# Kernel tuning notes

Hardware: AMD Instinct MI355X
Metric: run time of the kernel (lower is better)

## Reference

```python
import jax, jax.numpy as jnp
import numpy as np


def gcn_conv(x, src, dst, W, b, n_nodes):
    """PyG-style GCNConv: add self-loops, symmetric deg^-1/2 normalization,
    linear transform, scatter-add aggregation to dst, then bias."""
    loop = jnp.arange(n_nodes, dtype=src.dtype)
    s = jnp.concatenate([src, loop])
    d = jnp.concatenate([dst, loop])
    deg = jax.ops.segment_sum(jnp.ones_like(d, x.dtype), d, num_segments=n_nodes)
    dinv = jax.lax.rsqrt(deg)  # deg >= 1 due to self-loops
    norm = dinv[s] * dinv[d]  # [E+N]
    h = x @ W.T  # [N, out]
    msg = h[s] * norm[:, None]  # [E+N, out]
    return jax.ops.segment_sum(msg, d, num_segments=n_nodes) + b


def setup_inputs() -> dict:
    key = jax.random.key(0)
    k = jax.random.split(key, 6)
    N, E, IN, HID, OUT = 100000, 1600000, 128, 128, 64
    x = jax.random.normal(k[0], (N, IN), dtype=jnp.float32)
    edge_index = jax.random.randint(k[1], (2, E), 0, N, dtype=jnp.int64)
    W1 = jax.random.normal(k[2], (HID, IN), dtype=jnp.float32) * 0.05
    b1 = jnp.zeros((HID,), dtype=jnp.float32)
    W2 = jax.random.normal(k[3], (OUT, HID), dtype=jnp.float32) * 0.05
    b2 = jnp.zeros((OUT,), dtype=jnp.float32)
    return {"x": x, "W1": W1, "b1": b1, "W2": W2, "b2": b2, "edge_index": edge_index}


def reference(x, W1, b1, W2, b2, edge_index):
    n_nodes = x.shape[0]
    src, dst = edge_index[0], edge_index[1]
    h = jax.nn.relu(gcn_conv(x, src, dst, W1, b1, n_nodes))
    return gcn_conv(h, src, dst, W2, b2, n_nodes)
```

## Files before the change

kernel.cpp:

```cpp
#include <hip/hip_runtime.h>
#include <hip/hip_bf16.h>


#define IN_F  128
#define HID_F 128
#define OUT_F 64

#define NPB     128
#define MAXBKT  1024
#define CHUNK   2048
#define CAP     4096
#define SLAB    4096

typedef __bf16 bf16_t;
typedef __bf16 bf16x4 __attribute__((ext_vector_type(4)));
typedef __bf16 bf16x8 __attribute__((ext_vector_type(8)));
typedef float  f32x2  __attribute__((ext_vector_type(2)));
typedef float  f32x4  __attribute__((ext_vector_type(4)));
typedef unsigned u32x2 __attribute__((ext_vector_type(2)));
typedef unsigned u32x4 __attribute__((ext_vector_type(4)));

__global__ __launch_bounds__(256) void k_hist(const int* __restrict__ dst, int E,
                                              int* __restrict__ chunkhist, int NBKT,
                                              int pchunks,
                                              const float* __restrict__ W1s,
                                              const float* __restrict__ W2s,
                                              bf16_t* __restrict__ Wdst,
                                              int n1, int n2,
                                              int* __restrict__ bcur) {
    if ((int)blockIdx.x >= pchunks) {
        int i = (blockIdx.x - pchunks) * 256 + threadIdx.x;
        if (i < n1) Wdst[i] = (bf16_t)W1s[i];
        else if (i < n1 + n2) Wdst[i] = (bf16_t)W2s[i - n1];
        else if (i < n1 + n2 + NBKT) bcur[i - n1 - n2] = (i - n1 - n2) * SLAB;
        return;
    }
    __shared__ int cnt[MAXBKT];
    for (int i = threadIdx.x; i < NBKT; i += 256) cnt[i] = 0;
    __syncthreads();
    int base = blockIdx.x * CHUNK;
    for (int i = threadIdx.x; i < CHUNK; i += 256) {
        int e = base + i;
        if (e < E) atomicAdd(&cnt[dst[e] >> 7], 1);
    }
    __syncthreads();
    int* ch = chunkhist + (size_t)blockIdx.x * MAXBKT;
    for (int i = threadIdx.x; i < NBKT; i += 256) ch[i] = cnt[i];
}

__global__ __launch_bounds__(256) void k_part(const int* __restrict__ src,
                                              const int* __restrict__ dst, int E,
                                              int* __restrict__ bcur,
                                              const int* __restrict__ chunkhist,
                                              unsigned* __restrict__ part, int NBKT) {
    __shared__ int cnt[MAXBKT];
    __shared__ int base[MAXBKT];
    const int* ch = chunkhist + (size_t)blockIdx.x * MAXBKT;
    int off = (int)((blockIdx.x * 331u) % (unsigned)NBKT);
    for (int j = threadIdx.x; j < NBKT; j += 256) {
        int i = j + off; if (i >= NBKT) i -= NBKT;
        int c = ch[i];
        base[i] = c ? atomicAdd(&bcur[i], c) : 0;
        cnt[i] = 0;
    }
    __syncthreads();
    int cbase = blockIdx.x * CHUNK;
    for (int i = threadIdx.x; i < CHUNK; i += 256) {
        int e = cbase + i;
        if (e < E) {
            int d = dst[e];
            int b = d >> 7;
            int lp = atomicAdd(&cnt[b], 1);
            part[base[b] + lp] = (unsigned)src[e] | ((unsigned)(d & 127) << 17);
        }
    }
}

__global__ __launch_bounds__(256) void k_bucket(const unsigned* __restrict__ part,
                                                const int* __restrict__ bcur,
                                                int2* __restrict__ off2,
                                                int* __restrict__ col,
                                                float* __restrict__ dinv, int N) {
    __shared__ int lcnt[NPB];
    __shared__ int lexc[NPB];
    __shared__ int lcur[NPB];
    __shared__ int stage[CAP];
    int b = blockIdx.x;
    int t = threadIdx.x;
    int node0 = b * NPB;
    int nb = min(NPB, N - node0);
    int e0s = b * SLAB;
    int cnt = bcur[b] - e0s;
    if (t < NPB) lcnt[t] = 0;
    __syncthreads();
    for (int i = t; i < cnt; i += 256)
        atomicAdd(&lcnt[part[e0s + i] >> 17], 1);
    __syncthreads();
    if (t < NPB) lexc[t] = (lcnt[t] + 7) & ~7;
    __syncthreads();
    for (int ofs = 1; ofs < NPB; ofs <<= 1) {
        int add = (t >= ofs && t < NPB) ? lexc[t - ofs] : 0;
        __syncthreads();
        if (t < NPB) lexc[t] += add;
        __syncthreads();
    }
    if (t < NPB) {
        int pc = (lcnt[t] + 7) & ~7;
        int ex = lexc[t] - pc;
        lcur[t] = ex;
        if (t < nb) {
            off2[node0 + t] = make_int2(e0s + ex, e0s + ex + pc);
            dinv[node0 + t] = rsqrtf((float)lcnt[t] + 1.0f);
        }
    }
    __syncthreads();
    for (int i = t; i < cnt; i += 256) {
        unsigned p = part[e0s + i];
        int dl = p >> 17;
        int sv = (int)(p & 0x1FFFF);
        int lp = atomicAdd(&lcur[dl], 1);
        if (lp < CAP) stage[lp] = sv;
        else col[e0s + lp] = sv;
    }
    __syncthreads();
    if (t < NPB) {
        int en = lexc[t];
        for (int i = lcur[t]; i < en; i++) {
            if (i < CAP) stage[i] = N; else col[e0s + i] = N;
        }
    }
    __syncthreads();
    int tot = lexc[NPB - 1];
    for (int i = t; i < tot && i < CAP; i += 256) col[e0s + i] = stage[i];
}

template <int NCOL, typename TIN>
__global__ __launch_bounds__(256) void k_gemm_mfma(const TIN* __restrict__ X,
                                                   const bf16_t* __restrict__ W,
                                                   const float* __restrict__ scale,
                                                   bf16_t* __restrict__ H, int N) {
    constexpr int CT = NCOL / 16;
    int wv = threadIdx.x >> 6, lane = threadIdx.x & 63;
    int quad = lane >> 4, l16 = lane & 15;
    int row0 = blockIdx.x * 128 + wv * 32;
    f32x4 acc[2][CT] = {};
#pragma unroll
    for (int ks = 0; ks < 4; ks++) {
        int k0 = ks * 32 + quad * 8;
        bf16x8 a[2];
#pragma unroll
        for (int rt = 0; rt < 2; rt++) {
            int r = row0 + rt * 16 + l16;
            if (r >= N) r = N - 1;
            const TIN* p = X + (size_t)r * 128 + k0;
            if constexpr (sizeof(TIN) == 4) {
                f32x4 x0 = *(const f32x4*)p;
                f32x4 x1 = *(const f32x4*)(p + 4);
                bf16x8 tt;
                tt[0] = (bf16_t)x0[0]; tt[1] = (bf16_t)x0[1];
                tt[2] = (bf16_t)x0[2]; tt[3] = (bf16_t)x0[3];
                tt[4] = (bf16_t)x1[0]; tt[5] = (bf16_t)x1[1];
                tt[6] = (bf16_t)x1[2]; tt[7] = (bf16_t)x1[3];
                a[rt] = tt;
            } else {
                a[rt] = *(const bf16x8*)p;
            }
        }
#pragma unroll
        for (int ct = 0; ct < CT; ct++) {
            bf16x8 bfrag = *(const bf16x8*)(W + (size_t)(ct * 16 + l16) * 128 + k0);
#pragma unroll
            for (int rt = 0; rt < 2; rt++)
                acc[rt][ct] = __builtin_amdgcn_mfma_f32_16x16x32_bf16(a[rt], bfrag, acc[rt][ct], 0, 0, 0);
        }
    }
#pragma unroll
    for (int rt = 0; rt < 2; rt++)
#pragma unroll
        for (int r4 = 0; r4 < 4; r4++) {
            int r = row0 + rt * 16 + quad * 4 + r4;
            if (r < N) {
                float sc = scale[r];
#pragma unroll
                for (int ct = 0; ct < CT; ct++)
                    H[(size_t)r * NCOL + ct * 16 + l16] = (bf16_t)(sc * acc[rt][ct][r4]);
            } else if (r == N) {
#pragma unroll
                for (int ct = 0; ct < CT; ct++)
                    H[(size_t)N * NCOL + ct * 16 + l16] = (bf16_t)0.f;
            }
        }
}

template <int ROWE>
__device__ __forceinline__ void gather8(const bf16_t* __restrict__ hp,
                                        const int* __restrict__ col, int e,
                                        u32x4* w) {
    int4 c0 = *(const int4*)(col + e);
    int4 c1 = *(const int4*)(col + e + 4);
    w[0] = *(const u32x4*)(hp + (unsigned)c0.x * (unsigned)ROWE);
    w[1] = *(const u32x4*)(hp + (unsigned)c0.y * (unsigned)ROWE);
    w[2] = *(const u32x4*)(hp + (unsigned)c0.z * (unsigned)ROWE);
    w[3] = *(const u32x4*)(hp + (unsigned)c0.w * (unsigned)ROWE);
    w[4] = *(const u32x4*)(hp + (unsigned)c1.x * (unsigned)ROWE);
    w[5] = *(const u32x4*)(hp + (unsigned)c1.y * (unsigned)ROWE);
    w[6] = *(const u32x4*)(hp + (unsigned)c1.z * (unsigned)ROWE);
    w[7] = *(const u32x4*)(hp + (unsigned)c1.w * (unsigned)ROWE);
}

__device__ __forceinline__ void accum8(const u32x4* w, f32x2* a2) {
#pragma unroll
    for (int u = 0; u < 8; u++)
#pragma unroll
        for (int k = 0; k < 4; k++) {
            f32x2 v;
            v.x = __uint_as_float(w[u][k] << 16);
            v.y = __uint_as_float(w[u][k] & 0xffff0000u);
            a2[k] += v;
        }
}

__global__ __launch_bounds__(256) void k_agg_gemm(const bf16_t* __restrict__ h,
                                                  const int2* __restrict__ off2,
                                                  const int* __restrict__ col,
                                                  const float* __restrict__ dinv,
                                                  const float* __restrict__ bias,
                                                  const bf16_t* __restrict__ W2,
                                                  bf16_t* __restrict__ h2, int N) {
    __shared__ float hl[16][132];
    __shared__ float dl[16];
    int lane = threadIdx.x & 63;
    int wv = threadIdx.x >> 6;
    int g = lane >> 4, fl = lane & 15;
    int node0 = blockIdx.x * 16;
    int node = node0 + wv * 4 + g;
    bool alive = node < N;
    int f = fl * 8;
    const bf16_t* hp = h + f;
    f32x2 a2[4] = {};
    float di = 0.f;
    if (alive) {
        u32x4 ws = *(const u32x4*)(hp + (unsigned)node * 128u);
        int2 oe = off2[node];
        di = dinv[node];
#pragma unroll
        for (int k = 0; k < 4; k++) {
            f32x2 v;
            v.x = __uint_as_float(ws[k] << 16);
            v.y = __uint_as_float(ws[k] & 0xffff0000u);
            a2[k] = v;
        }
        u32x4 w[8];
        for (int e = oe.x; e < oe.y; e += 8) {
            gather8<128>(hp, col, e, w);
            accum8(w, a2);
        }
    }
    f32x4 b0 = *(const f32x4*)(bias + f);
    f32x4 b1 = *(const f32x4*)(bias + f + 4);
    int lr = wv * 4 + g;
#pragma unroll
    for (int j = 0; j < 8; j++) {
        float bv = (j < 4) ? b0[j] : b1[j - 4];
        float val = a2[j >> 1][j & 1] * di + bv;
        hl[lr][f + j] = fmaxf(val, 0.f);
    }
    if (fl == 0) dl[lr] = di;
    __syncthreads();

    int quad = lane >> 4, l16 = lane & 15;
    f32x4 c4 = {0.f, 0.f, 0.f, 0.f};
#pragma unroll
    for (int ks = 0; ks < 4; ks++) {
        int k0 = ks * 32 + quad * 8;
        bf16x8 afr;
#pragma unroll
        for (int j = 0; j < 8; j++) afr[j] = (bf16_t)hl[l16][k0 + j];
        bf16x8 bfr = *(const bf16x8*)(W2 + (size_t)(wv * 16 + l16) * 128 + k0);
        c4 = __builtin_amdgcn_mfma_f32_16x16x32_bf16(afr, bfr, c4, 0, 0, 0);
    }
#pragma unroll
    for (int r4 = 0; r4 < 4; r4++) {
        int rr = quad * 4 + r4;
        int gn = node0 + rr;
        if (gn < N)
            h2[(size_t)gn * 64 + wv * 16 + l16] = (bf16_t)(dl[rr] * c4[r4]);
    }
    if (blockIdx.x == 0 && threadIdx.x < 32)
        ((unsigned*)h2)[(size_t)N * 32 + threadIdx.x] = 0u;
}

template <int ROWE, int LPN, bool RELU, typename TOUT>
__global__ __launch_bounds__(256) void k_agg(const bf16_t* __restrict__ h,
                                             const int2* __restrict__ off2,
                                             const int* __restrict__ col,
                                             const float* __restrict__ dinv,
                                             const float* __restrict__ bias,
                                             TOUT* __restrict__ out, int N) {
    constexpr int NPW = 64 / LPN;
    int lane = threadIdx.x & 63;
    int wv = threadIdx.x >> 6;
    int g = lane / LPN, fl = lane % LPN;
    int node = blockIdx.x * (4 * NPW) + wv * NPW + g;
    if (node >= N) return;
    int f = fl * 8;
    const bf16_t* hp = h + f;
    u32x4 ws = *(const u32x4*)(hp + (unsigned)node * (unsigned)ROWE);
    int2 oe = off2[node];
    float di = dinv[node];
    f32x2 a2[4];
#pragma unroll
    for (int k = 0; k < 4; k++) {
        f32x2 v;
        v.x = __uint_as_float(ws[k] << 16);
        v.y = __uint_as_float(ws[k] & 0xffff0000u);
        a2[k] = v;
    }
    u32x4 w[8];
    for (int e = oe.x; e < oe.y; e += 8) {
        gather8<ROWE>(hp, col, e, w);
        accum8(w, a2);
    }
    f32x4 b0 = *(const f32x4*)(bias + f);
    f32x4 b1 = *(const f32x4*)(bias + f + 4);
    float r[8];
#pragma unroll
    for (int j = 0; j < 8; j++) {
        float bv = (j < 4) ? b0[j] : b1[j - 4];
        float val = a2[j >> 1][j & 1] * di + bv;
        if (RELU) val = fmaxf(val, 0.f);
        r[j] = val;
    }
    if constexpr (sizeof(TOUT) == 2) {
        bf16x8 v;
#pragma unroll
        for (int j = 0; j < 8; j++) v[j] = (bf16_t)r[j];
        *(bf16x8*)((bf16_t*)out + (size_t)node * ROWE + f) = v;
    } else {
        f32x4 v0 = {r[0], r[1], r[2], r[3]};
        f32x4 v1 = {r[4], r[5], r[6], r[7]};
        *(f32x4*)((float*)out + (size_t)node * ROWE + f) = v0;
        *(f32x4*)((float*)out + (size_t)node * ROWE + f + 4) = v1;
    }
}

extern "C" void kernel_launch(void* const* d_in, const int* in_sizes, int n_in,
                              void* d_out, int out_size, void* d_ws, size_t ws_size,
                              hipStream_t stream) {
    const float* x  = (const float*)d_in[0];
    const float* W1 = (const float*)d_in[1];
    const float* b1 = (const float*)d_in[2];
    const float* W2 = (const float*)d_in[3];
    const float* b2 = (const float*)d_in[4];
    const int*   ei = (const int*)d_in[5];

    int N = in_sizes[0] / IN_F;
    int E = in_sizes[5] / 2;
    const int* src = ei;
    const int* dst = ei + E;
    int NBKT = (N + NPB - 1) / NPB;
    int pchunks = (E + CHUNK - 1) / CHUNK;

    size_t woff = 0;
    auto alloc = [&](size_t bytes) {
        void* p = (char*)d_ws + woff;
        woff += (bytes + 255) & ~(size_t)255;
        return p;
    };
    int*      bcur  = (int*)alloc((size_t)NBKT * 4);
    int*      chist = (int*)alloc((size_t)pchunks * MAXBKT * 4);
    unsigned* part  = (unsigned*)alloc((size_t)NBKT * SLAB * 4);
    int*      col   = (int*)alloc((size_t)NBKT * SLAB * 4);
    int2*     off2  = (int2*)alloc((size_t)N * 8);
    float*    dinv  = (float*)alloc((size_t)N * 4);
    bf16_t*   Wb    = (bf16_t*)alloc((size_t)(HID_F * IN_F + OUT_F * HID_F) * 2);
    bf16_t*   W1b   = Wb;
    bf16_t*   W2b   = Wb + HID_F * IN_F;
    bf16_t*   h1    = (bf16_t*)alloc((size_t)(N + 1) * HID_F * 2);
    bf16_t*   h2b   = (bf16_t*)alloc((size_t)(N + 1) * OUT_F * 2);
    float*    outp  = (float*)d_out;

    int n1 = HID_F * IN_F, n2 = OUT_F * HID_F;
    int tailblocks = (n1 + n2 + NBKT + 255) / 256;
    k_hist<<<pchunks + tailblocks, 256, 0, stream>>>(dst, E, chist, NBKT, pchunks,
                                                     W1, W2, Wb, n1, n2, bcur);
    k_part<<<pchunks, 256, 0, stream>>>(src, dst, E, bcur, chist, part, NBKT);
    k_bucket<<<NBKT, 256, 0, stream>>>(part, bcur, off2, col, dinv, N);

    int gemm_blocks = (N + 127) / 128;

    k_gemm_mfma<HID_F, float><<<gemm_blocks, 256, 0, stream>>>(x, W1b, dinv, h1, N);
    k_agg_gemm<<<(N + 15) / 16, 256, 0, stream>>>(h1, off2, col, dinv, b1, W2b, h2b, N);
    k_agg<OUT_F, 8, false, float><<<(N + 31) / 32, 256, 0, stream>>>(h2b, off2, col, dinv, b2, outp, N);
}
```

Baseline: 268.3 us.

## Use larger 512-node buckets with padded bucket cursors in CSR build

Bucket granularity grows from 128 to 512 destination nodes, so there are fewer buckets and larger edge chunks and slabs. The per-bucket cursor counters are spaced 16 ints apart to avoid atomic contention on shared cache lines. The bucket kernel's prefix scan now handles two nodes per thread. The aim is to reduce per-block overhead in the histogram, partition and bucket kernels. In exchange each bucket kernel block carries a much larger LDS stage buffer, which may lower occupancy, and there are fewer blocks in the grid.

```diff
diff --git a/kernel.cpp b/kernel.cpp
--- a/kernel.cpp
+++ b/kernel.cpp
@@ -6,11 +6,11 @@
 #define HID_F 128
 #define OUT_F 64
 
-#define NPB     128
-#define MAXBKT  1024
-#define CHUNK   2048
-#define CAP     4096
-#define SLAB    4096
+#define NPB     512
+#define MAXBKT  256
+#define CHUNK   4096
+#define SLAB    12288
+#define CAP     12288
 
 typedef __bf16 bf16_t;
 typedef __bf16 bf16x4 __attribute__((ext_vector_type(4)));
@@ -32,7 +32,7 @@
         int i = (blockIdx.x - pchunks) * 256 + threadIdx.x;
         if (i < n1) Wdst[i] = (bf16_t)W1s[i];
         else if (i < n1 + n2) Wdst[i] = (bf16_t)W2s[i - n1];
-        else if (i < n1 + n2 + NBKT) bcur[i - n1 - n2] = (i - n1 - n2) * SLAB;
+        else if (i < n1 + n2 + NBKT) bcur[(i - n1 - n2) * 16] = (i - n1 - n2) * SLAB;
         return;
     }
     __shared__ int cnt[MAXBKT];
@@ -41,7 +41,7 @@
     int base = blockIdx.x * CHUNK;
     for (int i = threadIdx.x; i < CHUNK; i += 256) {
         int e = base + i;
-        if (e < E) atomicAdd(&cnt[dst[e] >> 7], 1);
+        if (e < E) atomicAdd(&cnt[dst[e] >> 9], 1);
     }
     __syncthreads();
     int* ch = chunkhist + (size_t)blockIdx.x * MAXBKT;
@@ -56,11 +56,11 @@
     __shared__ int cnt[MAXBKT];
     __shared__ int base[MAXBKT];
     const int* ch = chunkhist + (size_t)blockIdx.x * MAXBKT;
-    int off = (int)((blockIdx.x * 331u) % (unsigned)NBKT);
+    int off = (int)((blockIdx.x * 73u) % (unsigned)NBKT);
     for (int j = threadIdx.x; j < NBKT; j += 256) {
         int i = j + off; if (i >= NBKT) i -= NBKT;
         int c = ch[i];
-        base[i] = c ? atomicAdd(&bcur[i], c) : 0;
+        base[i] = c ? atomicAdd(&bcur[i * 16], c) : 0;
         cnt[i] = 0;
     }
     __syncthreads();
@@ -69,9 +69,9 @@
         int e = cbase + i;
         if (e < E) {
             int d = dst[e];
-            int b = d >> 7;
+            int b = d >> 9;
             int lp = atomicAdd(&cnt[b], 1);
-            part[base[b] + lp] = (unsigned)src[e] | ((unsigned)(d & 127) << 17);
+            part[base[b] + lp] = (unsigned)src[e] | ((unsigned)(d & 511) << 17);
         }
     }
 }
@@ -84,33 +84,43 @@
     __shared__ int lcnt[NPB];
     __shared__ int lexc[NPB];
     __shared__ int lcur[NPB];
+    __shared__ int psum[256];
     __shared__ int stage[CAP];
     int b = blockIdx.x;
     int t = threadIdx.x;
     int node0 = b * NPB;
-    int nb = min(NPB, N - node0);
     int e0s = b * SLAB;
-    int cnt = bcur[b] - e0s;
-    if (t < NPB) lcnt[t] = 0;
+    int cnt = bcur[b * 16] - e0s;
+    for (int i = t; i < NPB; i += 256) lcnt[i] = 0;
     __syncthreads();
     for (int i = t; i < cnt; i += 256)
         atomicAdd(&lcnt[part[e0s + i] >> 17], 1);
     __syncthreads();
-    if (t < NPB) lexc[t] = (lcnt[t] + 7) & ~7;
-    __syncthreads();
-    for (int ofs = 1; ofs < NPB; ofs <<= 1) {
-        int add = (t >= ofs && t < NPB) ? lexc[t - ofs] : 0;
+    int n2b = t * 2;
+    int pc0 = (lcnt[n2b] + 7) & ~7;
+    int pc1 = (lcnt[n2b + 1] + 7) & ~7;
+    psum[t] = pc0 + pc1;
+    __syncthreads();
+    for (int ofs = 1; ofs < 256; ofs <<= 1) {
+        int add = (t >= ofs) ? psum[t - ofs] : 0;
         __syncthreads();
-        if (t < NPB) lexc[t] += add;
+        psum[t] += add;
         __syncthreads();
     }
-    if (t < NPB) {
-        int pc = (lcnt[t] + 7) & ~7;
-        int ex = lexc[t] - pc;
-        lcur[t] = ex;
-        if (t < nb) {
-            off2[node0 + t] = make_int2(e0s + ex, e0s + ex + pc);
-            dinv[node0 + t] = rsqrtf((float)lcnt[t] + 1.0f);
+    int run = (t > 0) ? psum[t - 1] : 0;
+    {
+        lexc[n2b] = run; lcur[n2b] = run;
+        int node = node0 + n2b;
+        if (node < N) {
+            off2[node] = make_int2(e0s + run, e0s + run + pc0);
+            dinv[node] = rsqrtf((float)lcnt[n2b] + 1.0f);
+        }
+        run += pc0;
+        lexc[n2b + 1] = run; lcur[n2b + 1] = run;
+        node = node0 + n2b + 1;
+        if (node < N) {
+            off2[node] = make_int2(e0s + run, e0s + run + pc1);
+            dinv[node] = rsqrtf((float)lcnt[n2b + 1] + 1.0f);
         }
     }
     __syncthreads();
@@ -123,14 +133,16 @@
         else col[e0s + lp] = sv;
     }
     __syncthreads();
-    if (t < NPB) {
-        int en = lexc[t];
-        for (int i = lcur[t]; i < en; i++) {
+#pragma unroll
+    for (int j = 0; j < 2; j++) {
+        int idx = n2b + j;
+        int en = lexc[idx] + ((lcnt[idx] + 7) & ~7);
+        for (int i = lcur[idx]; i < en; i++) {
             if (i < CAP) stage[i] = N; else col[e0s + i] = N;
         }
     }
     __syncthreads();
-    int tot = lexc[NPB - 1];
+    int tot = psum[255];
     for (int i = t; i < tot && i < CAP; i += 256) col[e0s + i] = stage[i];
 }
 
@@ -367,7 +379,7 @@
         woff += (bytes + 255) & ~(size_t)255;
         return p;
     };
-    int*      bcur  = (int*)alloc((size_t)NBKT * 4);
+    int*      bcur  = (int*)alloc((size_t)NBKT * 16 * 4);
     int*      chist = (int*)alloc((size_t)pchunks * MAXBKT * 4);
     unsigned* part  = (unsigned*)alloc((size_t)NBKT * SLAB * 4);
     int*      col   = (int*)alloc((size_t)NBKT * SLAB * 4);
```

New measurement: 266.2 us. Within noise of the previous version (-0.8%).
